# Optimization experiments

Hardware: AMD Instinct MI355X
Metric: run time of the kernel (lower is better)

Reference implementation:

```python
import jax, jax.numpy as jnp
import numpy as np

STATE_BITS = 10          # L: bits of trellis state
SHIFT_BITS = 2           # K: bits shifted in per step -> 2^K predecessors
CHUNK = 4                # chunk_size: values emitted per trellis step
S = 1 << STATE_BITS      # number of states (codebook rows)
NPRED = 1 << SHIFT_BITS  # predecessors per state
HI = 1 << (STATE_BITS - SHIFT_BITS)


def setup_inputs() -> dict:
    key = jax.random.key(0)
    k1, k2 = jax.random.split(key)
    array = jax.random.normal(k1, (1024, 1024), dtype=jnp.float32)
    codebook = jax.random.normal(k2, (S, CHUNK), dtype=jnp.float32)
    return {"array": array, "codebook": codebook, "block_size": 16}


def _viterbi(x, codebook):
    # x: [T, CHUNK, B] target chunks; codebook: [S, CHUNK]
    # Exact min-squared-error Viterbi over the bit-shift trellis:
    #   next_state = ((prev << K) | new_bits) mod 2^L
    # Predecessors of state s: (s >> K) + j * 2^(L-K), j in [0, 2^K)
    s = jnp.arange(S)
    prev_idx = (s[:, None] >> SHIFT_BITS) + jnp.arange(NPRED)[None, :] * HI  # [S, NPRED]
    cnorm = jnp.sum(codebook * codebook, axis=1)  # [S]

    def cost(xt):  # xt: [CHUNK, B] -> [S, B] squared distances
        return cnorm[:, None] - 2.0 * (codebook @ xt) + jnp.sum(xt * xt, axis=0)[None, :]

    alpha0 = cost(x[0])  # free initial state: cost of emitting first chunk

    def step(alpha, xt):
        cand = alpha[prev_idx]                        # [S, NPRED, B]
        j = jnp.argmin(cand, axis=1)                  # [S, B]
        alpha_new = jnp.min(cand, axis=1) + cost(xt)  # [S, B]
        return alpha_new, j.astype(jnp.int8)

    alpha_T, bps = jax.lax.scan(step, alpha0, x[1:])  # bps: [T-1, S, B] int8
    last = jnp.argmin(alpha_T, axis=0).astype(jnp.int32)  # [B] state at step T-1

    def back(state, bp):
        # state: [B] state at step t; bp: [S, B] backpointers into step t
        j = jnp.take_along_axis(bp, state[None, :], axis=0)[0].astype(jnp.int32)
        prev = (state >> SHIFT_BITS) + j * HI
        return prev, state

    first, rest = jax.lax.scan(back, last, bps, reverse=True)
    return jnp.concatenate([first[None], rest], axis=0)  # [T, B] int32


def reference(array, codebook, block_size):
    rows, columns = array.shape
    br, bc = rows // block_size, columns // block_size
    epb = block_size * block_size          # elements_per_block
    T = epb // CHUNK                       # number_of_steps
    B = br * bc                            # number_of_blocks
    # block reshape: [rows, cols] -> [elements_per_block, number_of_blocks]
    blocks = (array.reshape(br, block_size, bc, block_size)
                   .transpose(0, 2, 1, 3)
                   .reshape(B, epb).T)
    x = blocks.reshape(T, CHUNK, B)
    states = _viterbi(x, codebook)         # [T, B]
    vals = codebook[states]                # [T, B, CHUNK] gather reconstruct
    rec = vals.transpose(0, 2, 1).reshape(epb, B)
    rec = (rec.T.reshape(br, bc, block_size, block_size)
              .transpose(0, 2, 1, 3)
              .reshape(rows, columns))
    states_out = states.T.reshape(br, bc, T)
    return rec, states_out
```

## Files before the change

### kernel.cpp

```cpp
#include <hip/hip_runtime.h>


#define COLS      1024
#define T_STEPS   64
#define REC_SIZE  (1024 * 1024)

__global__ __launch_bounds__(128) void viterbi_q(
    const float* __restrict__ arr,
    const float* __restrict__ cbook,
    float* __restrict__ out)
{
    const int tid   = threadIdx.x;
    const int wid   = tid >> 6;
    const int lane  = tid & 63;
    const int chain = blockIdx.x;
    const int rb    = chain >> 6;
    const int cbc   = chain & 63;

    __shared__ __align__(16) float tile[256];
    __shared__ __align__(16) float Mbuf[512];
    __shared__ unsigned char J[32 * 128];
    __shared__ int   st_lds[64];
    __shared__ float redv[2];
    __shared__ int   reds[2];

    if (tid < 64) {
        const int r  = tid >> 2;
        const int c4 = (tid & 3) << 2;
        float4 v = *(const float4*)(arr + (rb * 16 + r) * COLS + cbc * 16 + c4);
        *(float4*)&tile[tid << 2] = v;
    }
    *(float2*)&Mbuf[tid << 1] = make_float2(0.f, 0.f);

    float4 a[8];
    float  h[8];
    #pragma unroll
    for (int j = 0; j < 4; ++j) {
        #pragma unroll
        for (int c = 0; c < 2; ++c) {
            const int row = (tid << 1) + c + (j << 8);
            float4 v = *(const float4*)(cbook + row * 4);
            a[j * 2 + c] = v;
            h[j * 2 + c] = -0.5f * (v.x * v.x + v.y * v.y +
                                    v.z * v.z + v.w * v.w);
        }
    }
    __syncthreads();

    const int pg = tid >> 1;
    unsigned nib_hold = 0;

    #pragma unroll 1
    for (int t = 0; t < T_STEPS - 1; ++t) {
        const float* __restrict__ Mr = Mbuf + ((t & 1) << 8);
        float* __restrict__       Mw = Mbuf + (((t + 1) & 1) << 8);

        float4 xt = *(const float4*)&tile[t << 2];
        float mj[4];
        #pragma unroll
        for (int j = 0; j < 4; ++j)
            mj[j] = Mr[pg + 64 * j];

        float nm[2];
        unsigned bp = 0;
        #pragma unroll
        for (int c = 0; c < 2; ++c) {
            float cand[4];
            #pragma unroll
            for (int j = 0; j < 4; ++j) {
                const float4 av = a[j * 2 + c];
                float acc = fmaf(av.x, xt.x, h[j * 2 + c]);
                acc = fmaf(av.y, xt.y, acc);
                acc = fmaf(av.z, xt.z, acc);
                acc = fmaf(av.w, xt.w, acc);
                cand[c ? 4 + j - 4 : j] = acc + mj[j];
                cand[j] = acc + mj[j];
            }
            const float v = fmaxf(fmaxf(cand[0], cand[1]),
                                  fmaxf(cand[2], cand[3]));
            const int j = (cand[0] == v) ? 0
                        : (cand[1] == v) ? 1
                        : (cand[2] == v) ? 2 : 3;
            nm[c] = v;
            bp |= (unsigned)j << (2 * c);
        }
        *(float2*)&Mw[tid << 1] = make_float2(nm[0], nm[1]);
        if (t & 1) J[(t >> 1) * 128 + tid] = (unsigned char)(nib_hold | (bp << 4));
        else       nib_hold = bp;
        __syncthreads();
    }
    J[31 * 128 + tid] = (unsigned char)nib_hold;

    {
        const float* __restrict__ Mr = Mbuf + ((63 & 1) << 8);
        float4 xt = *(const float4*)&tile[63 << 2];
        float mj[4];
        #pragma unroll
        for (int j = 0; j < 4; ++j)
            mj[j] = Mr[pg + 64 * j];

        float bv = -3.4e38f;
        int   bs = 0;
        #pragma unroll
        for (int j = 0; j < 4; ++j) {
            #pragma unroll
            for (int c = 0; c < 2; ++c) {
                const float4 av = a[j * 2 + c];
                float acc = fmaf(av.x, xt.x, h[j * 2 + c]);
                acc = fmaf(av.y, xt.y, acc);
                acc = fmaf(av.z, xt.z, acc);
                acc = fmaf(av.w, xt.w, acc);
                acc += mj[j];
                if (acc > bv) { bv = acc; bs = (tid << 1) + c + (j << 8); }
            }
        }
        #pragma unroll
        for (int off = 32; off > 0; off >>= 1) {
            const float ov = __shfl_xor(bv, off, 64);
            const int   os = __shfl_xor(bs, off, 64);
            if (ov > bv || (ov == bv && os < bs)) { bv = ov; bs = os; }
        }
        if (lane == 0) { redv[wid] = bv; reds[wid] = bs; }
    }
    __syncthreads();

    if (tid == 0) {
        float bv = redv[0]; int bs = reds[0];
        if (redv[1] > bv || (redv[1] == bv && reds[1] < bs)) {
            bv = redv[1]; bs = reds[1];
        }
        int s = bs;
        st_lds[T_STEPS - 1] = s;
        for (int i = T_STEPS - 2; i >= 0; --i) {
            const int p = s >> 2;
            const unsigned byte = J[(i >> 1) * 128 + (p >> 1)];
            const int j = (byte >> (((i & 1) << 2) + ((p & 1) << 1))) & 3;
            s = p + (j << 8);
            st_lds[i] = s;
        }
    }
    __syncthreads();

    if (tid < 64) {
        const int st = st_lds[tid];
        const float4 v = *(const float4*)(cbook + st * 4);
        const int r  = tid >> 2;
        const int c4 = (tid & 3) << 2;
        *(float4*)(out + (rb * 16 + r) * COLS + cbc * 16 + c4) = v;
    } else {
        const int t = tid - 64;
        out[REC_SIZE + chain * 64 + t] = (float)st_lds[t];
    }
}

extern "C" void kernel_launch(void* const* d_in, const int* in_sizes, int n_in,
                              void* d_out, int out_size, void* d_ws, size_t ws_size,
                              hipStream_t stream)
{
    const float* arr   = (const float*)d_in[0];
    const float* cbook = (const float*)d_in[1];
    float* out = (float*)d_out;
    viterbi_q<<<dim3(4096), dim3(128), 0, stream>>>(arr, cbook, out);
}
```

Baseline: 107.7 us.

## Use one thread per state with packed v2f FMAs and 4-step backpointer packing

Doubles the block to 256 threads so each thread owns one trellis state instead of two, and computes its four predecessor candidates with packed two-wide FMAs. Backpointers for four steps are packed into one byte per state, and the step loop is partially unrolled. The aim is a shorter per-step critical path between barriers in this latency-bound recursion. In exchange it doubles thread count and barrier participants per block, which may lower blocks per CU.

```diff
diff --git a/kernel.cpp b/kernel.cpp
--- a/kernel.cpp
+++ b/kernel.cpp
@@ -1,11 +1,13 @@
 #include <hip/hip_runtime.h>
 
+
+typedef float v2f __attribute__((ext_vector_type(2)));
 
 #define COLS      1024
 #define T_STEPS   64
 #define REC_SIZE  (1024 * 1024)
 
-__global__ __launch_bounds__(128) void viterbi_q(
+__global__ __launch_bounds__(256) void viterbi_q(
     const float* __restrict__ arr,
     const float* __restrict__ cbook,
     float* __restrict__ out)
@@ -18,11 +20,11 @@
     const int cbc   = chain & 63;
 
     __shared__ __align__(16) float tile[256];
-    __shared__ __align__(16) float Mbuf[512];
-    __shared__ unsigned char J[32 * 128];
+    __shared__ __align__(16) float Mbuf[2][256];
+    __shared__ unsigned char J[16 * 256];
     __shared__ int   st_lds[64];
-    __shared__ float redv[2];
-    __shared__ int   reds[2];
+    __shared__ float redv[4];
+    __shared__ int   reds[4];
 
     if (tid < 64) {
         const int r  = tid >> 2;
@@ -30,90 +32,87 @@
         float4 v = *(const float4*)(arr + (rb * 16 + r) * COLS + cbc * 16 + c4);
         *(float4*)&tile[tid << 2] = v;
     }
-    *(float2*)&Mbuf[tid << 1] = make_float2(0.f, 0.f);
+    Mbuf[0][tid] = 0.f;
 
-    float4 a[8];
-    float  h[8];
-    #pragma unroll
-    for (int j = 0; j < 4; ++j) {
-        #pragma unroll
-        for (int c = 0; c < 2; ++c) {
-            const int row = (tid << 1) + c + (j << 8);
-            float4 v = *(const float4*)(cbook + row * 4);
-            a[j * 2 + c] = v;
-            h[j * 2 + c] = -0.5f * (v.x * v.x + v.y * v.y +
-                                    v.z * v.z + v.w * v.w);
-        }
+    v2f ax01, ay01, az01, aw01, h01;
+    v2f ax23, ay23, az23, aw23, h23;
+    {
+        float4 r0 = *(const float4*)(cbook + (tid       ) * 4);
+        float4 r1 = *(const float4*)(cbook + (tid +  256) * 4);
+        float4 r2 = *(const float4*)(cbook + (tid +  512) * 4);
+        float4 r3 = *(const float4*)(cbook + (tid +  768) * 4);
+        ax01 = (v2f){r0.x, r1.x}; ay01 = (v2f){r0.y, r1.y};
+        az01 = (v2f){r0.z, r1.z}; aw01 = (v2f){r0.w, r1.w};
+        ax23 = (v2f){r2.x, r3.x}; ay23 = (v2f){r2.y, r3.y};
+        az23 = (v2f){r2.z, r3.z}; aw23 = (v2f){r2.w, r3.w};
+        h01 = (v2f){ -0.5f*(r0.x*r0.x + r0.y*r0.y + r0.z*r0.z + r0.w*r0.w),
+                     -0.5f*(r1.x*r1.x + r1.y*r1.y + r1.z*r1.z + r1.w*r1.w) };
+        h23 = (v2f){ -0.5f*(r2.x*r2.x + r2.y*r2.y + r2.z*r2.z + r2.w*r2.w),
+                     -0.5f*(r3.x*r3.x + r3.y*r3.y + r3.z*r3.z + r3.w*r3.w) };
     }
     __syncthreads();
 
-    const int pg = tid >> 1;
-    unsigned nib_hold = 0;
+    const int bq = tid >> 2;
+    unsigned nib = 0;
 
+    auto step = [&](int t) {
+        const float* __restrict__ Mr = Mbuf[t & 1];
+        float* __restrict__       Mw = Mbuf[(t + 1) & 1];
+        float4 xt = *(const float4*)&tile[t << 2];
+        const float m0 = Mr[bq], m1 = Mr[bq + 64],
+                    m2 = Mr[bq + 128], m3 = Mr[bq + 192];
+        v2f acc01 = h01, acc23 = h23;
+        const v2f xx = (v2f){xt.x, xt.x}, yy = (v2f){xt.y, xt.y},
+                  zz = (v2f){xt.z, xt.z}, ww = (v2f){xt.w, xt.w};
+        acc01 = __builtin_elementwise_fma(ax01, xx, acc01);
+        acc23 = __builtin_elementwise_fma(ax23, xx, acc23);
+        acc01 = __builtin_elementwise_fma(ay01, yy, acc01);
+        acc23 = __builtin_elementwise_fma(ay23, yy, acc23);
+        acc01 = __builtin_elementwise_fma(az01, zz, acc01);
+        acc23 = __builtin_elementwise_fma(az23, zz, acc23);
+        acc01 = __builtin_elementwise_fma(aw01, ww, acc01);
+        acc23 = __builtin_elementwise_fma(aw23, ww, acc23);
+        const v2f c01 = acc01 + (v2f){m0, m1};
+        const v2f c23 = acc23 + (v2f){m2, m3};
+        const v2f vm  = __builtin_elementwise_max(c01, c23);
+        const float v = fmaxf(vm.x, vm.y);
+        const int j = (c01.x == v) ? 0
+                    : (c01.y == v) ? 1
+                    : (c23.x == v) ? 2 : 3;
+        Mw[tid] = v;
+        nib |= (unsigned)j << ((t & 3) * 2);
+        if ((t & 3) == 3) { J[(t >> 2) * 256 + tid] = (unsigned char)nib; nib = 0; }
+        __syncthreads();
+    };
+
+    #pragma unroll 4
+    for (int t = 0; t < 60; ++t) step(t);
     #pragma unroll 1
-    for (int t = 0; t < T_STEPS - 1; ++t) {
-        const float* __restrict__ Mr = Mbuf + ((t & 1) << 8);
-        float* __restrict__       Mw = Mbuf + (((t + 1) & 1) << 8);
-
-        float4 xt = *(const float4*)&tile[t << 2];
-        float mj[4];
-        #pragma unroll
-        for (int j = 0; j < 4; ++j)
-            mj[j] = Mr[pg + 64 * j];
-
-        float nm[2];
-        unsigned bp = 0;
-        #pragma unroll
-        for (int c = 0; c < 2; ++c) {
-            float cand[4];
-            #pragma unroll
-            for (int j = 0; j < 4; ++j) {
-                const float4 av = a[j * 2 + c];
-                float acc = fmaf(av.x, xt.x, h[j * 2 + c]);
-                acc = fmaf(av.y, xt.y, acc);
-                acc = fmaf(av.z, xt.z, acc);
-                acc = fmaf(av.w, xt.w, acc);
-                cand[c ? 4 + j - 4 : j] = acc + mj[j];
-                cand[j] = acc + mj[j];
-            }
-            const float v = fmaxf(fmaxf(cand[0], cand[1]),
-                                  fmaxf(cand[2], cand[3]));
-            const int j = (cand[0] == v) ? 0
-                        : (cand[1] == v) ? 1
-                        : (cand[2] == v) ? 2 : 3;
-            nm[c] = v;
-            bp |= (unsigned)j << (2 * c);
-        }
-        *(float2*)&Mw[tid << 1] = make_float2(nm[0], nm[1]);
-        if (t & 1) J[(t >> 1) * 128 + tid] = (unsigned char)(nib_hold | (bp << 4));
-        else       nib_hold = bp;
-        __syncthreads();
-    }
-    J[31 * 128 + tid] = (unsigned char)nib_hold;
+    for (int t = 60; t < 63; ++t) step(t);
+    J[15 * 256 + tid] = (unsigned char)nib;
 
     {
-        const float* __restrict__ Mr = Mbuf + ((63 & 1) << 8);
+        const float* __restrict__ Mr = Mbuf[63 & 1];
         float4 xt = *(const float4*)&tile[63 << 2];
-        float mj[4];
-        #pragma unroll
-        for (int j = 0; j < 4; ++j)
-            mj[j] = Mr[pg + 64 * j];
-
-        float bv = -3.4e38f;
-        int   bs = 0;
-        #pragma unroll
-        for (int j = 0; j < 4; ++j) {
-            #pragma unroll
-            for (int c = 0; c < 2; ++c) {
-                const float4 av = a[j * 2 + c];
-                float acc = fmaf(av.x, xt.x, h[j * 2 + c]);
-                acc = fmaf(av.y, xt.y, acc);
-                acc = fmaf(av.z, xt.z, acc);
-                acc = fmaf(av.w, xt.w, acc);
-                acc += mj[j];
-                if (acc > bv) { bv = acc; bs = (tid << 1) + c + (j << 8); }
-            }
-        }
+        const float m0 = Mr[bq], m1 = Mr[bq + 64],
+                    m2 = Mr[bq + 128], m3 = Mr[bq + 192];
+        v2f acc01 = h01, acc23 = h23;
+        const v2f xx = (v2f){xt.x, xt.x}, yy = (v2f){xt.y, xt.y},
+                  zz = (v2f){xt.z, xt.z}, ww = (v2f){xt.w, xt.w};
+        acc01 = __builtin_elementwise_fma(ax01, xx, acc01);
+        acc23 = __builtin_elementwise_fma(ax23, xx, acc23);
+        acc01 = __builtin_elementwise_fma(ay01, yy, acc01);
+        acc23 = __builtin_elementwise_fma(ay23, yy, acc23);
+        acc01 = __builtin_elementwise_fma(az01, zz, acc01);
+        acc23 = __builtin_elementwise_fma(az23, zz, acc23);
+        acc01 = __builtin_elementwise_fma(aw01, ww, acc01);
+        acc23 = __builtin_elementwise_fma(aw23, ww, acc23);
+        const float cv0 = acc01.x + m0, cv1 = acc01.y + m1;
+        const float cv2 = acc23.x + m2, cv3 = acc23.y + m3;
+        float bv = cv0; int bs = tid;
+        if (cv1 > bv) { bv = cv1; bs = tid + 256; }
+        if (cv2 > bv) { bv = cv2; bs = tid + 512; }
+        if (cv3 > bv) { bv = cv3; bs = tid + 768; }
         #pragma unroll
         for (int off = 32; off > 0; off >>= 1) {
             const float ov = __shfl_xor(bv, off, 64);
@@ -126,15 +125,17 @@
 
     if (tid == 0) {
         float bv = redv[0]; int bs = reds[0];
-        if (redv[1] > bv || (redv[1] == bv && reds[1] < bs)) {
-            bv = redv[1]; bs = reds[1];
-        }
+        #pragma unroll
+        for (int w = 1; w < 4; ++w)
+            if (redv[w] > bv || (redv[w] == bv && reds[w] < bs)) {
+                bv = redv[w]; bs = reds[w];
+            }
         int s = bs;
         st_lds[T_STEPS - 1] = s;
         for (int i = T_STEPS - 2; i >= 0; --i) {
             const int p = s >> 2;
-            const unsigned byte = J[(i >> 1) * 128 + (p >> 1)];
-            const int j = (byte >> (((i & 1) << 2) + ((p & 1) << 1))) & 3;
+            const unsigned byte = J[(i >> 2) * 256 + p];
+            const int j = (byte >> ((i & 3) * 2)) & 3;
             s = p + (j << 8);
             st_lds[i] = s;
         }
@@ -147,7 +148,7 @@
         const int r  = tid >> 2;
         const int c4 = (tid & 3) << 2;
         *(float4*)(out + (rb * 16 + r) * COLS + cbc * 16 + c4) = v;
-    } else {
+    } else if (tid < 128) {
         const int t = tid - 64;
         out[REC_SIZE + chain * 64 + t] = (float)st_lds[t];
     }
@@ -160,5 +161,5 @@
     const float* arr   = (const float*)d_in[0];
     const float* cbook = (const float*)d_in[1];
     float* out = (float*)d_out;
-    viterbi_q<<<dim3(4096), dim3(128), 0, stream>>>(arr, cbook, out);
+    viterbi_q<<<dim3(4096), dim3(256), 0, stream>>>(arr, cbook, out);
 }
```

Result: no change. 109.5 us (+1.7%).
